# Performance work log

Measured on AMD Instinct MI355X. Metric: run time of the kernel, lower is better.

The kernel has to match this reference:

```python
import jax, jax.numpy as jnp
import numpy as np


def _layernorm(x, w, b):
    mu = x.mean(-1, keepdims=True)
    var = ((x - mu) ** 2).mean(-1, keepdims=True)
    return (x - mu) * jax.lax.rsqrt(var + 1e-5) * w + b


def _s5_scan(u, Lam, Bc, Cc, D, log_step):
    # Diagonal S5 SSM, ZOH discretization, parallel associative scan over time.
    step = jnp.exp(log_step)                       # (P,)
    Lbar = jnp.exp(Lam * step)                     # (P,) complex
    Bbar = ((Lbar - 1.0) / Lam)[:, None] * Bc      # (P,H) complex
    Bu = jnp.einsum('ph,blh->blp', Bbar, u.astype(Bbar.dtype))  # (B,L,P)
    Le = jnp.broadcast_to(Lbar, Bu.shape)

    def binop(e1, e2):
        a1, b1 = e1
        a2, b2 = e2
        return a1 * a2, a2 * b1 + b2

    _, xs = jax.lax.associative_scan(binop, (Le, Bu), axis=1)   # hidden states (B,L,P)
    return 2.0 * jnp.einsum('hp,blp->blh', Cc, xs).real + D * u


def _s5_block(x, ln1_w, ln1_b, Lam_re, Lam_im, B_re, B_im, C_re, C_im, D, log_step,
              ln2_w, ln2_b, ff_enc_w, ff_dec_w):
    # S5Block.forward (dropout = identity at inference)
    fx = _layernorm(x, ln1_w, ln1_b)
    Lam = -jnp.exp(Lam_re) + 1j * Lam_im           # stable-real parametrization
    y = _s5_scan(fx, Lam, B_re + 1j * B_im, C_re + 1j * C_im, D, log_step)
    x = jax.nn.gelu(y, approximate=False) + fx
    fx = _layernorm(x, ln2_w, ln2_b)
    h = fx @ ff_enc_w                              # (B,L,2N) -> GEGLU
    v, g = jnp.split(h, 2, axis=-1)
    h = v * jax.nn.gelu(g, approximate=False)
    return h @ ff_dec_w + fx


def reference(z_input, dt, ln1_w, ln1_b, Lam_re, Lam_im, B_re, B_im, C_re, C_im, D,
              log_step, ln2_w, ln2_b, ff_enc_w, ff_dec_w, toA_w1, toA_b1, toA_w2,
              toA_b2, mask_A):
    Bsz, L, N = z_input.shape
    x = z_input
    for i in range(ln1_w.shape[0]):                # n_ssmlayer_A stacked S5 blocks
        x = _s5_block(x, ln1_w[i], ln1_b[i], Lam_re[i], Lam_im[i], B_re[i], B_im[i],
                      C_re[i], C_im[i], D[i], log_step[i], ln2_w[i], ln2_b[i],
                      ff_enc_w[i], ff_dec_w[i])
    # ssm_to_A: Linear -> Softplus -> Linear
    h = jax.nn.softplus(x @ toA_w1 + toA_b1)
    Unk_A = h @ toA_w2 + toA_b2                    # (B,L,N*N)
    # SSM_step_ODE.get_seq_dynamics with A_known_const = 0
    A = Unk_A.reshape(Bsz, L, N, N) * mask_A
    # bilinear (Tustin) discretization: A_bar = (I - dt/2 A)^-1 (I + dt/2 A)
    I = jnp.eye(N, dtype=A.dtype)
    dtA = 0.5 * dt[..., None, None] * A
    A_bar = jnp.linalg.solve(I - dtA, I + dtA)     # (B,L,N,N)
    # roll latent state through the discretized dynamics
    z0 = z_input[:, 0]

    def step(z, Ab):
        z2 = jnp.einsum('bij,bj->bi', Ab, z)
        return z2, z2

    _, ys = jax.lax.scan(step, z0, jnp.moveaxis(A_bar[:, :-1], 1, 0))
    traj = jnp.concatenate([z0[None], ys], axis=0)  # (L,B,N)
    return jnp.moveaxis(traj, 0, 1)                 # (B,L,N)


def setup_inputs() -> dict:
    key = jax.random.key(0)
    ks = jax.random.split(key, 16)
    B, L, N, P, NL, H = 32, 512, 64, 128, 2, 128
    d = {}
    d['z_input'] = jax.random.normal(ks[0], (B, L, N), jnp.float32)
    d['dt'] = jax.random.uniform(ks[1], (B, L), jnp.float32) * 0.01
    d['ln1_w'] = jnp.ones((NL, N), jnp.float32)
    d['ln1_b'] = jnp.zeros((NL, N), jnp.float32)
    d['Lam_re'] = jax.random.normal(ks[2], (NL, P), jnp.float32) * 0.5
    d['Lam_im'] = jax.random.normal(ks[3], (NL, P), jnp.float32) * np.pi
    d['B_re'] = jax.random.normal(ks[4], (NL, P, N), jnp.float32) / np.sqrt(N)
    d['B_im'] = jax.random.normal(ks[5], (NL, P, N), jnp.float32) / np.sqrt(N)
    d['C_re'] = jax.random.normal(ks[6], (NL, N, P), jnp.float32) / np.sqrt(P)
    d['C_im'] = jax.random.normal(ks[7], (NL, N, P), jnp.float32) / np.sqrt(P)
    d['D'] = jax.random.normal(ks[8], (NL, N), jnp.float32)
    lo, hi = np.log(1e-3), np.log(1e-1)
    d['log_step'] = lo + jax.random.uniform(ks[9], (NL, P), jnp.float32) * (hi - lo)
    d['ln2_w'] = jnp.ones((NL, N), jnp.float32)
    d['ln2_b'] = jnp.zeros((NL, N), jnp.float32)
    d['ff_enc_w'] = jax.random.normal(ks[10], (NL, N, 2 * N), jnp.float32) / np.sqrt(N)
    d['ff_dec_w'] = jax.random.normal(ks[11], (NL, N, N), jnp.float32) / np.sqrt(N)
    d['toA_w1'] = jax.random.normal(ks[12], (N, H), jnp.float32) * 0.1
    d['toA_b1'] = jnp.zeros((H,), jnp.float32)
    d['toA_w2'] = jax.random.normal(ks[13], (H, N * N), jnp.float32) * 0.002
    d['toA_b2'] = jnp.zeros((N * N,), jnp.float32)
    d['mask_A'] = jnp.ones((N, N), jnp.float32)
    return d
```

## Files before the change

### kernel.cpp

```cpp
#include <hip/hip_runtime.h>

#define DI __device__ __forceinline__

typedef unsigned short u16;
typedef unsigned int u32;
typedef __attribute__((ext_vector_type(8))) short shortx8;
typedef __attribute__((ext_vector_type(4))) float floatx4;

DI float u2f(u32 x) { union { u32 u; float f; } v; v.u = x; return v.f; }
DI u32 f2u(float x) { union { u32 u; float f; } v; v.f = x; return v.u; }
DI float bflo(u32 w) { return u2f(w << 16); }
DI float bfhi(u32 w) { return u2f(w & 0xffff0000u); }
DI float bf1(u16 w) { return u2f(((u32)w) << 16); }
DI u16 f2bf(float f) {
  u32 u = f2u(f);
  u32 r = (u + 0x7fffu + ((u >> 16) & 1u)) >> 16;
  return (u16)r;
}

DI float wsum64(float v) {
  v += __shfl_xor(v, 32);
  v += __shfl_xor(v, 16);
  v += __shfl_xor(v, 8);
  v += __shfl_xor(v, 4);
  v += __shfl_xor(v, 2);
  v += __shfl_xor(v, 1);
  return v;
}

DI float gelu_ex(float y) { return 0.5f * y * (1.0f + erff(y * 0.7071067811865476f)); }
DI float softplus_ex(float x) { return x > 0.f ? x + log1pf(expf(-x)) : log1pf(expf(x)); }

__global__ __launch_bounds__(256) void k_pre2(
    const float* __restrict__ Lam_re, const float* __restrict__ Lam_im,
    const float* __restrict__ log_step,
    const float* __restrict__ B_re, const float* __restrict__ B_im,
    const float* __restrict__ C_re, const float* __restrict__ C_im,
    const float* __restrict__ w2,
    float* __restrict__ wLbar, float* __restrict__ wBbr, float* __restrict__ wBbi,
    float* __restrict__ wCtr, float* __restrict__ wCti, u16* __restrict__ w2T) {
  if (blockIdx.x < 64) {
    __shared__ float s[128][65];
    int t = threadIdx.x;
    int n0 = blockIdx.x * 64;
    for (int i = 0; i < 32; ++i) {
      int e = i * 256 + t;
      int k = e >> 6, n = e & 63;
      s[k][n] = w2[(size_t)k * 4096 + n0 + n];
    }
    __syncthreads();
    for (int i = 0; i < 16; ++i) {
      int e = i * 256 + t;
      int n = e >> 6, kp = e & 63;
      u32 pk = (u32)f2bf(s[kp * 2][n]) | ((u32)f2bf(s[kp * 2 + 1][n]) << 16);
      ((u32*)w2T)[(size_t)(n0 + n) * 64 + kp] = pk;
    }
  } else {
    int l = blockIdx.x - 64;
    int p = threadIdx.x;
    if (p < 128) {
      int idx = l * 128 + p;
      float step = expf(log_step[idx]);
      float lre = -expf(Lam_re[idx]);
      float lim = Lam_im[idx];
      float er = expf(lre * step);
      float Lr = er * cosf(lim * step);
      float Li = er * sinf(lim * step);
      wLbar[idx * 2] = Lr;
      wLbar[idx * 2 + 1] = Li;
      float inv = 1.0f / (lre * lre + lim * lim);
      float nr = Lr - 1.0f, ni = Li;
      float qr = (nr * lre + ni * lim) * inv;
      float qi = (ni * lre - nr * lim) * inv;
      for (int h = 0; h < 64; ++h) {
        float br = B_re[idx * 64 + h], bim = B_im[idx * 64 + h];
        wBbr[(l * 64 + h) * 128 + p] = qr * br - qi * bim;
        wBbi[(l * 64 + h) * 128 + p] = qr * bim + qi * br;
        wCtr[idx * 64 + h] = C_re[(l * 64 + h) * 128 + p];
        wCti[idx * 64 + h] = C_im[(l * 64 + h) * 128 + p];
      }
    }
  }
}

__global__ __launch_bounds__(256) void k_ln_bu(
    const float* __restrict__ xin, const float* __restrict__ lnw, const float* __restrict__ lnb,
    const float* __restrict__ wBbr, const float* __restrict__ wBbi,
    float* __restrict__ fxg, float2* __restrict__ bu, int layer) {
  __shared__ float sbr[64 * 128];
  __shared__ float sbi[64 * 128];
  int t = threadIdx.x, w = t >> 6, lane = t & 63;
  {
    const float* br = wBbr + (size_t)layer * 8192;
    const float* bi = wBbi + (size_t)layer * 8192;
    for (int e = t; e < 8192; e += 256) { sbr[e] = br[e]; sbi[e] = bi[e]; }
  }
  float wv = lnw[layer * 64 + lane], bv = lnb[layer * 64 + lane];
  __syncthreads();
  int row0 = blockIdx.x * 32 + w * 8;
  float fxv[8];
#pragma unroll
  for (int rr = 0; rr < 8; ++rr) {
    size_t r = row0 + rr;
    float x = xin[r * 64 + lane];
    float mu = wsum64(x) * 0.015625f;
    float d = x - mu;
    float var = wsum64(d * d) * 0.015625f;
    float fx = d * rsqrtf(var + 1e-5f) * wv + bv;
    fxv[rr] = fx;
    fxg[r * 64 + lane] = fx;
  }
  float ar0[8] = {}, ai0[8] = {}, ar1[8] = {}, ai1[8] = {};
  for (int h = 0; h < 64; ++h) {
    float b0r = sbr[h * 128 + lane], b0i = sbi[h * 128 + lane];
    float b1r = sbr[h * 128 + lane + 64], b1i = sbi[h * 128 + lane + 64];
#pragma unroll
    for (int rr = 0; rr < 8; ++rr) {
      float f = __shfl(fxv[rr], h);
      ar0[rr] = fmaf(b0r, f, ar0[rr]);
      ai0[rr] = fmaf(b0i, f, ai0[rr]);
      ar1[rr] = fmaf(b1r, f, ar1[rr]);
      ai1[rr] = fmaf(b1i, f, ai1[rr]);
    }
  }
#pragma unroll
  for (int rr = 0; rr < 8; ++rr) {
    size_t r = row0 + rr;
    bu[r * 128 + lane] = make_float2(ar0[rr], ai0[rr]);
    bu[r * 128 + lane + 64] = make_float2(ar1[rr], ai1[rr]);
  }
}

__global__ __launch_bounds__(256) void k_scan(float2* __restrict__ bu,
                                              const float* __restrict__ wLbar, int layer) {
  __shared__ float2 carry[16][17];
  int t = threadIdx.x;
  int ck = t >> 4, chain = t & 15;
  int b = blockIdx.x >> 3;
  int p = (blockIdx.x & 7) * 16 + chain;
  float Lr = wLbar[(layer * 128 + p) * 2];
  float Li = wLbar[(layer * 128 + p) * 2 + 1];
  float2* ptr = bu + ((size_t)b * 512 * 128 + p);
  int l0 = ck * 32;
  float xr = 0.f, xi = 0.f;
#pragma unroll 4
  for (int i = 0; i < 32; ++i) {
    float2 v = ptr[(size_t)(l0 + i) * 128];
    float nr = fmaf(Lr, xr, fmaf(-Li, xi, v.x));
    float ni = fmaf(Lr, xi, fmaf(Li, xr, v.y));
    xr = nr; xi = ni;
  }
  carry[chain][ck] = make_float2(xr, xi);
  __syncthreads();
  if (t < 16) {
    float ar = Lr, ai = Li;
#pragma unroll
    for (int s = 0; s < 5; ++s) {
      float nr = ar * ar - ai * ai;
      float ni = 2.f * ar * ai;
      ar = nr; ai = ni;
    }
    float cr = 0.f, ci2 = 0.f;
#pragma unroll
    for (int m = 0; m < 16; ++m) {
      float2 loc = carry[t][m];
      carry[t][m] = make_float2(cr, ci2);
      float nr = fmaf(ar, cr, fmaf(-ai, ci2, loc.x));
      float ni = fmaf(ar, ci2, fmaf(ai, cr, loc.y));
      cr = nr; ci2 = ni;
    }
  }
  __syncthreads();
  float2 c0 = carry[chain][ck];
  xr = c0.x; xi = c0.y;
#pragma unroll 4
  for (int i = 0; i < 32; ++i) {
    float2 v = ptr[(size_t)(l0 + i) * 128];
    float nr = fmaf(Lr, xr, fmaf(-Li, xi, v.x));
    float ni = fmaf(Lr, xi, fmaf(Li, xr, v.y));
    xr = nr; xi = ni;
    ptr[(size_t)(l0 + i) * 128] = make_float2(xr, xi);
  }
}

__global__ __launch_bounds__(256) void k_yff(
    const float2* __restrict__ xs, const float* __restrict__ wCtr, const float* __restrict__ wCti,
    const float* __restrict__ fxg, const float* __restrict__ Dp,
    const float* __restrict__ ln2w, const float* __restrict__ ln2b,
    const float* __restrict__ encw, const float* __restrict__ decw,
    const float* __restrict__ w1, const float* __restrict__ b1,
    float* __restrict__ xout, u16* __restrict__ h1out, int layer) {
  __shared__ union {
    struct { float ctr[4096]; float cti[4096]; float2 xsh[4][8][64]; } a;
    struct { float enc[8192]; float dec[4096]; } b;
    struct { float w1s[8192]; } c;
  } sm;
  int t = threadIdx.x, w = t >> 6, lane = t & 63;
  int row0 = blockIdx.x * 32 + w * 8;
  float acc[8] = {};
  for (int ph = 0; ph < 2; ++ph) {
    __syncthreads();
    {
      const float* sr = wCtr + ((size_t)layer * 128 + ph * 64) * 64;
      const float* si = wCti + ((size_t)layer * 128 + ph * 64) * 64;
      for (int e = t; e < 4096; e += 256) { sm.a.ctr[e] = sr[e]; sm.a.cti[e] = si[e]; }
    }
#pragma unroll
    for (int rr = 0; rr < 8; ++rr) {
      size_t r = row0 + rr;
      sm.a.xsh[w][rr][lane] = xs[r * 128 + ph * 64 + lane];
    }
    __syncthreads();
    for (int p = 0; p < 64; ++p) {
      float cr = sm.a.ctr[p * 64 + lane];
      float ci = sm.a.cti[p * 64 + lane];
#pragma unroll
      for (int rr = 0; rr < 8; ++rr) {
        float2 xv = sm.a.xsh[w][rr][p];
        acc[rr] = fmaf(cr, xv.x, fmaf(-ci, xv.y, acc[rr]));
      }
    }
  }
  float Dv = Dp[layer * 64 + lane];
  float xv[8];
#pragma unroll
  for (int rr = 0; rr < 8; ++rr) {
    size_t r = row0 + rr;
    float u = fxg[r * 64 + lane];
    float y = 2.f * acc[rr] + Dv * u;
    xv[rr] = gelu_ex(y) + u;
  }
  __syncthreads();
  {
    const float* e = encw + (size_t)layer * 8192;
    for (int i = t; i < 8192; i += 256) sm.b.enc[i] = e[i];
    const float* d = decw + (size_t)layer * 4096;
    for (int i = t; i < 4096; i += 256) sm.b.dec[i] = d[i];
  }
  float wv = ln2w[layer * 64 + lane], bv = ln2b[layer * 64 + lane];
  __syncthreads();
  float fx2v[8];
#pragma unroll
  for (int rr = 0; rr < 8; ++rr) {
    float x = xv[rr];
    float mu = wsum64(x) * 0.015625f;
    float d = x - mu;
    float var = wsum64(d * d) * 0.015625f;
    fx2v[rr] = d * rsqrtf(var + 1e-5f) * wv + bv;
  }
  float h0[8] = {}, h1v[8] = {};
  for (int h = 0; h < 64; ++h) {
    float e0 = sm.b.enc[h * 128 + lane], e1 = sm.b.enc[h * 128 + lane + 64];
#pragma unroll
    for (int rr = 0; rr < 8; ++rr) {
      float f = __shfl(fx2v[rr], h);
      h0[rr] = fmaf(e0, f, h0[rr]);
      h1v[rr] = fmaf(e1, f, h1v[rr]);
    }
  }
  float gv[8];
#pragma unroll
  for (int rr = 0; rr < 8; ++rr) gv[rr] = h0[rr] * gelu_ex(h1v[rr]);
  float x2[8];
  {
    float o[8] = {};
    for (int j = 0; j < 64; ++j) {
      float dv = sm.b.dec[j * 64 + lane];
#pragma unroll
      for (int rr = 0; rr < 8; ++rr) {
        float gj = __shfl(gv[rr], j);
        o[rr] = fmaf(dv, gj, o[rr]);
      }
    }
#pragma unroll
    for (int rr = 0; rr < 8; ++rr) x2[rr] = o[rr] + fx2v[rr];
  }
  if (layer == 0) {
#pragma unroll
    for (int rr = 0; rr < 8; ++rr) xout[(size_t)(row0 + rr) * 64 + lane] = x2[rr];
    return;
  }
  __syncthreads();
  for (int i = t; i < 8192; i += 256) sm.c.w1s[i] = w1[i];
  float bb0 = b1[lane], bb1 = b1[lane + 64];
  __syncthreads();
  float a0[8] = {}, a1[8] = {};
  for (int h = 0; h < 64; ++h) {
    float e0 = sm.c.w1s[h * 128 + lane], e1 = sm.c.w1s[h * 128 + lane + 64];
#pragma unroll
    for (int rr = 0; rr < 8; ++rr) {
      float f = __shfl(x2[rr], h);
      a0[rr] = fmaf(e0, f, a0[rr]);
      a1[rr] = fmaf(e1, f, a1[rr]);
    }
  }
#pragma unroll
  for (int rr = 0; rr < 8; ++rr) {
    size_t r = row0 + rr;
    float v0 = softplus_ex(a0[rr] + bb0);
    float v1 = softplus_ex(a1[rr] + bb1);
    int sl = (2 * lane) & 63;
    float ea = __shfl(v0, sl), eb = __shfl(v1, sl);
    float oa = __shfl(v0, sl + 1), ob = __shfl(v1, sl + 1);
    float lo = (lane < 32) ? ea : eb;
    float hi = (lane < 32) ? oa : ob;
    ((u32*)h1out)[r * 64 + lane] = (u32)f2bf(lo) | ((u32)f2bf(hi) << 16);
  }
}

__global__ __launch_bounds__(256) void k_gemm_mfma(
    const u16* __restrict__ w2T, const u16* __restrict__ h1,
    const float* __restrict__ b2, const float* __restrict__ mask,
    const float* __restrict__ dt, u16* __restrict__ Xout) {
  __shared__ __align__(16) u16 As[128 * 128];
  __shared__ __align__(16) u16 Bs[128 * 128];
  int t = threadIdx.x;
  int bn = blockIdx.x;
  int bm = blockIdx.y;
  {
    const u16* srcA = w2T + (size_t)(bn * 128) * 128;
    const u16* srcB = h1 + (size_t)(bm * 128) * 128;
#pragma unroll
    for (int i = 0; i < 8; ++i) {
      int r = i * 16 + (t >> 4);
      int gs = t & 15;
      int gsw = (gs & 8) | ((gs ^ r) & 7);
      uint4 va = *(const uint4*)(srcA + r * 128 + gs * 8);
      *(uint4*)(As + r * 128 + gsw * 8) = va;
      uint4 vb = *(const uint4*)(srcB + r * 128 + gs * 8);
      *(uint4*)(Bs + r * 128 + gsw * 8) = vb;
    }
  }
  __syncthreads();
  int w = t >> 6, l = t & 63;
  int n0 = (w & 1) * 64, m0 = (w >> 1) * 64;
  int lr = l & 15, kg = l >> 4;
  floatx4 acc[4][4];
#pragma unroll
  for (int i = 0; i < 4; ++i)
#pragma unroll
    for (int j = 0; j < 4; ++j) acc[i][j] = (floatx4){0.f, 0.f, 0.f, 0.f};
#pragma unroll
  for (int kk = 0; kk < 4; ++kk) {
    int g = kk * 4 + kg;
    shortx8 af[4], bf[4];
#pragma unroll
    for (int ni = 0; ni < 4; ++ni) {
      int r = n0 + ni * 16 + lr;
      int gsw = (g & 8) | ((g ^ r) & 7);
      af[ni] = *(const shortx8*)(As + r * 128 + gsw * 8);
    }
#pragma unroll
    for (int mi = 0; mi < 4; ++mi) {
      int r = m0 + mi * 16 + lr;
      int gsw = (g & 8) | ((g ^ r) & 7);
      bf[mi] = *(const shortx8*)(Bs + r * 128 + gsw * 8);
    }
#pragma unroll
    for (int ni = 0; ni < 4; ++ni)
#pragma unroll
      for (int mi = 0; mi < 4; ++mi)
        acc[ni][mi] = __builtin_amdgcn_mfma_f32_16x16x32_bf16(af[ni], bf[mi], acc[ni][mi], 0, 0, 0);
  }
  __syncthreads();
  int q = (l >> 4) * 4;
#pragma unroll
  for (int mi = 0; mi < 4; ++mi) {
    int ml = m0 + mi * 16 + lr;
    int m = bm * 128 + ml;
    float dv = 0.5f * dt[m];
#pragma unroll
    for (int ni = 0; ni < 4; ++ni) {
      int nl = n0 + ni * 16 + q;
      int n = bn * 128 + nl;
      float4 bb = *(const float4*)&b2[n];
      float4 mk = *(const float4*)&mask[n];
      floatx4 a = acc[ni][mi];
      float x0 = dv * (a[0] + bb.x) * mk.x;
      float x1 = dv * (a[1] + bb.y) * mk.y;
      float x2 = dv * (a[2] + bb.z) * mk.z;
      float x3 = dv * (a[3] + bb.w) * mk.w;
      u32 lo = (u32)f2bf(x0) | ((u32)f2bf(x1) << 16);
      u32 hi = (u32)f2bf(x2) | ((u32)f2bf(x3) << 16);
      int g = nl >> 3;
      int gsw = (g & 8) | ((g ^ ml) & 7);
      *(uint2*)(As + ml * 128 + gsw * 8 + (nl & 7)) = make_uint2(lo, hi);
    }
  }
  __syncthreads();
  int seg = t & 7;
#pragma unroll
  for (int pp = 0; pp < 4; ++pp) {
    int r = pp * 32 + (t >> 3);
#pragma unroll
    for (int ii = 0; ii < 2; ++ii) {
      int g = seg * 2 + ii;
      int gsw = (g & 8) | ((g ^ r) & 7);
      uint4 v = *(const uint4*)(As + r * 128 + gsw * 8);
      *(uint4*)&Xout[(size_t)(bm * 128 + r) * 4096 + bn * 128 + g * 8] = v;
    }
  }
}

__global__ __launch_bounds__(256, 4) void k_chunk(u16* __restrict__ Xg) {
  __shared__ __align__(16) u16 Xrm[4096];
  __shared__ __align__(16) u16 XTrm[4096];
  __shared__ __align__(16) u16 Erm[4096];
  __shared__ __align__(16) u16 STb[4096];
  __shared__ __align__(16) u16 SOut[4096];
  int t = threadIdx.x, w = t >> 6, l = t & 63;
  int lr = l & 15, kg = l >> 4;
  int b = blockIdx.x >> 5, c = blockIdx.x & 31;
  u16* base = Xg + ((size_t)(b * 512 + c * 16)) * 4096;
  floatx4 sreg[4];
#pragma unroll
  for (int i = 0; i < 4; ++i) sreg[i] = (floatx4){0.f, 0.f, 0.f, 0.f};
  int r0 = (t >> 3) * 2, c0 = (t & 7) * 8, g0 = t & 7;
  int cw = t >> 3;
  uint4 pf0 = *(const uint4*)(base + r0 * 64 + c0);
  uint4 pf1 = *(const uint4*)(base + (r0 + 1) * 64 + c0);
  int q0 = w * 16 + kg * 4;
  int qrow = w * 16 + lr;
  int wr = t >> 2, wg = (t & 3) * 2;
  for (int j = 0; j < 16; ++j) {
    __syncthreads();
    if (j > 0) {
      u16* Xprev = base + (size_t)(j - 1) * 4096;
      uint4 v0 = *(const uint4*)(SOut + wr * 64 + (((wg + 0) ^ wr) & 7) * 8);
      uint4 v1 = *(const uint4*)(SOut + wr * 64 + (((wg + 1) ^ wr) & 7) * 8);
      *(uint4*)(Xprev + wr * 64 + wg * 8) = v0;
      *(uint4*)(Xprev + wr * 64 + wg * 8 + 8) = v1;
    }
    *(uint4*)(Xrm + r0 * 64 + ((g0 ^ r0) & 7) * 8) = pf0;
    *(uint4*)(Xrm + (r0 + 1) * 64 + ((g0 ^ (r0 + 1)) & 7) * 8) = pf1;
    {
      const u16* a = (const u16*)&pf0;
      const u16* bq = (const u16*)&pf1;
#pragma unroll
      for (int i = 0; i < 8; ++i) {
        int ci = (i + t) & 7;
        int cc = c0 + ci;
        u32 val = (u32)a[ci] | ((u32)bq[ci] << 16);
        ((u32*)XTrm)[cc * 32 + (((cw >> 2) ^ cc) & 7) * 4 + (cw & 3)] = val;
      }
    }
#pragma unroll
    for (int j2 = 0; j2 < 4; ++j2) {
      int p = j2 * 16 + lr;
      floatx4 s = sreg[j2];
      float v0 = s[0] + ((p == q0 + 0) ? 1.f : 0.f);
      float v1 = s[1] + ((p == q0 + 1) ? 1.f : 0.f);
      float v2 = s[2] + ((p == q0 + 2) ? 1.f : 0.f);
      float v3 = s[3] + ((p == q0 + 3) ? 1.f : 0.f);
      u32 lo = (u32)f2bf(v0) | ((u32)f2bf(v1) << 16);
      u32 hi = (u32)f2bf(v2) | ((u32)f2bf(v3) << 16);
      *(uint2*)(STb + p * 64 + (((q0 >> 3) ^ p) & 7) * 8 + (q0 & 7)) = make_uint2(lo, hi);
    }
    if (j < 15) {
      const u16* nx = base + (size_t)(j + 1) * 4096;
      pf0 = *(const uint4*)(nx + r0 * 64 + c0);
      pf1 = *(const uint4*)(nx + (r0 + 1) * 64 + c0);
    }
    __syncthreads();
    shortx8 afx0 = *(const shortx8*)(XTrm + qrow * 64 + ((kg ^ qrow) & 7) * 8);
    shortx8 afx1 = *(const shortx8*)(XTrm + qrow * 64 + (((4 + kg) ^ qrow) & 7) * 8);
    {
      floatx4 acc[4];
#pragma unroll
      for (int i = 0; i < 4; ++i) acc[i] = (floatx4){0.f, 0.f, 0.f, 0.f};
#pragma unroll
      for (int kk = 0; kk < 2; ++kk) {
        int g = kk * 4 + kg;
        shortx8 af = kk ? afx1 : afx0;
#pragma unroll
        for (int j2 = 0; j2 < 4; ++j2) {
          int p = j2 * 16 + lr;
          shortx8 bf = *(const shortx8*)(Xrm + p * 64 + ((g ^ p) & 7) * 8);
          acc[j2] = __builtin_amdgcn_mfma_f32_16x16x32_bf16(af, bf, acc[j2], 0, 0, 0);
        }
      }
#pragma unroll
      for (int j2 = 0; j2 < 4; ++j2) {
        int p = j2 * 16 + lr;
        int sw = (((q0 >> 3) ^ p) & 7) * 8 + (q0 & 7);
        uint2 xv = *(const uint2*)(Xrm + p * 64 + sw);
        floatx4 a = acc[j2];
        float e0 = 2.f * (bflo(xv.x) + a[0]);
        float e1 = 2.f * (bfhi(xv.x) + a[1]);
        float e2 = 2.f * (bflo(xv.y) + a[2]);
        float e3 = 2.f * (bfhi(xv.y) + a[3]);
        u32 lo = (u32)f2bf(e0) | ((u32)f2bf(e1) << 16);
        u32 hi = (u32)f2bf(e2) | ((u32)f2bf(e3) << 16);
        *(uint2*)(Erm + p * 64 + sw) = make_uint2(lo, hi);
      }
    }
    __syncthreads();
    {
      floatx4 acc[4];
#pragma unroll
      for (int i = 0; i < 4; ++i) acc[i] = (floatx4){0.f, 0.f, 0.f, 0.f};
#pragma unroll
      for (int kk = 0; kk < 2; ++kk) {
        int g = kk * 4 + kg;
        shortx8 af = *(const shortx8*)(Erm + qrow * 64 + ((g ^ qrow) & 7) * 8);
#pragma unroll
        for (int j2 = 0; j2 < 4; ++j2) {
          int p = j2 * 16 + lr;
          shortx8 bf = *(const shortx8*)(STb + p * 64 + ((g ^ p) & 7) * 8);
          acc[j2] = __builtin_amdgcn_mfma_f32_16x16x32_bf16(af, bf, acc[j2], 0, 0, 0);
        }
      }
#pragma unroll
      for (int j2 = 0; j2 < 4; ++j2) {
        int p = j2 * 16 + lr;
        floatx4 a = acc[j2];
        floatx4 s = sreg[j2];
        s[0] += a[0]; s[1] += a[1]; s[2] += a[2]; s[3] += a[3];
        sreg[j2] = s;
#pragma unroll
        for (int i = 0; i < 4; ++i) {
          int r2 = q0 + i;
          SOut[r2 * 64 + (((p >> 3) ^ r2) & 7) * 8 + (p & 7)] = f2bf(s[i]);
        }
      }
    }
  }
  __syncthreads();
  {
    u16* Xprev = base + (size_t)15 * 4096;
    uint4 v0 = *(const uint4*)(SOut + wr * 64 + (((wg + 0) ^ wr) & 7) * 8);
    uint4 v1 = *(const uint4*)(SOut + wr * 64 + (((wg + 1) ^ wr) & 7) * 8);
    *(uint4*)(Xprev + wr * 64 + wg * 8) = v0;
    *(uint4*)(Xprev + wr * 64 + wg * 8 + 8) = v1;
  }
}

__global__ __launch_bounds__(64) void k_carry(const float* __restrict__ zin,
                                              const u16* __restrict__ R,
                                              float* __restrict__ out) {
  int b = blockIdx.x, l = threadIdx.x;
  uint4 cf[8], nf[8];
  {
    const uint4* M0 = (const uint4*)(R + ((size_t)(b * 512 + 15)) * 4096 + l * 64);
#pragma unroll
    for (int g = 0; g < 8; ++g) cf[g] = M0[g];
  }
  float cz = zin[(size_t)b * 512 * 64 + l];
  for (int c = 0; c < 32; ++c) {
    out[((size_t)(b * 512 + c * 16)) * 64 + l] = cz;
    if (c < 31) {
      const uint4* Mn = (const uint4*)(R + ((size_t)(b * 512 + (c + 1) * 16 + 15)) * 4096 + l * 64);
#pragma unroll
      for (int g = 0; g < 8; ++g) nf[g] = Mn[g];
    }
    float a0 = 0.f, a1 = 0.f, a2 = 0.f, a3 = 0.f;
#pragma unroll
    for (int g = 0; g < 8; ++g) {
      uint4 v = cf[g];
      int k = g * 8;
      a0 = fmaf(bflo(v.x), __shfl(cz, k + 0), a0);
      a1 = fmaf(bfhi(v.x), __shfl(cz, k + 1), a1);
      a2 = fmaf(bflo(v.y), __shfl(cz, k + 2), a2);
      a3 = fmaf(bfhi(v.y), __shfl(cz, k + 3), a3);
      a0 = fmaf(bflo(v.z), __shfl(cz, k + 4), a0);
      a1 = fmaf(bfhi(v.z), __shfl(cz, k + 5), a1);
      a2 = fmaf(bflo(v.w), __shfl(cz, k + 6), a2);
      a3 = fmaf(bfhi(v.w), __shfl(cz, k + 7), a3);
    }
    cz += (a0 + a1) + (a2 + a3);
    if (c < 31) {
#pragma unroll
      for (int g = 0; g < 8; ++g) cf[g] = nf[g];
    }
  }
}

__global__ __launch_bounds__(256) void k_apply(const u16* __restrict__ R,
                                               float* __restrict__ out) {
  __shared__ float carr[64];
  int t = threadIdx.x, w = t >> 6, l = t & 63;
  int b = blockIdx.x >> 5, c = blockIdx.x & 31;
  const u16* Rb = R + ((size_t)(b * 512 + c * 16)) * 4096;
  if (t < 64) carr[t] = out[((size_t)(b * 512 + c * 16)) * 64 + t];
  __syncthreads();
  float zl = carr[l];
  for (int j = w; j < 15; j += 4) {
    const uint4* M = (const uint4*)(Rb + (size_t)j * 4096 + l * 64);
    float a0 = 0.f, a1 = 0.f, a2 = 0.f, a3 = 0.f;
#pragma unroll
    for (int g = 0; g < 8; ++g) {
      uint4 v = M[g];
      const float* zb = &carr[g * 8];
      a0 = fmaf(bflo(v.x), zb[0], a0);
      a1 = fmaf(bfhi(v.x), zb[1], a1);
      a2 = fmaf(bflo(v.y), zb[2], a2);
      a3 = fmaf(bfhi(v.y), zb[3], a3);
      a0 = fmaf(bflo(v.z), zb[4], a0);
      a1 = fmaf(bfhi(v.z), zb[5], a1);
      a2 = fmaf(bflo(v.w), zb[6], a2);
      a3 = fmaf(bfhi(v.w), zb[7], a3);
    }
    out[((size_t)(b * 512 + c * 16 + j + 1)) * 64 + l] = zl + ((a0 + a1) + (a2 + a3));
  }
}

extern "C" void kernel_launch(void* const* d_in, const int* in_sizes, int n_in,
                              void* d_out, int out_size, void* d_ws, size_t ws_size,
                              hipStream_t stream) {
  const float* z_input  = (const float*)d_in[0];
  const float* dt       = (const float*)d_in[1];
  const float* ln1_w    = (const float*)d_in[2];
  const float* ln1_b    = (const float*)d_in[3];
  const float* Lam_re   = (const float*)d_in[4];
  const float* Lam_im   = (const float*)d_in[5];
  const float* B_re     = (const float*)d_in[6];
  const float* B_im     = (const float*)d_in[7];
  const float* C_re     = (const float*)d_in[8];
  const float* C_im     = (const float*)d_in[9];
  const float* Dp       = (const float*)d_in[10];
  const float* log_step = (const float*)d_in[11];
  const float* ln2_w    = (const float*)d_in[12];
  const float* ln2_b    = (const float*)d_in[13];
  const float* ff_enc   = (const float*)d_in[14];
  const float* ff_dec   = (const float*)d_in[15];
  const float* toA_w1   = (const float*)d_in[16];
  const float* toA_b1   = (const float*)d_in[17];
  const float* toA_w2   = (const float*)d_in[18];
  const float* toA_b2   = (const float*)d_in[19];
  const float* mask_A   = (const float*)d_in[20];

  char* ws = (char*)d_ws;
  float* wLbar = (float*)(ws + 0);
  float* wBbr  = (float*)(ws + 2048);
  float* wBbi  = (float*)(ws + 67584);
  float* wCtr  = (float*)(ws + 133120);
  float* wCti  = (float*)(ws + 198656);
  float* wfx   = (float*)(ws + 264192);
  float* wx    = (float*)(ws + 4458496);
  float2* wbu  = (float2*)(ws + 8652800);
  u16* wh1     = (u16*)(ws + 25430016);
  u16* w2T     = (u16*)(ws + 29624320);
  u16* wX      = (u16*)(ws + 30672896);
  if (ws_size < 164890624ull) return;

  k_pre2<<<66, 256, 0, stream>>>(Lam_re, Lam_im, log_step, B_re, B_im, C_re, C_im,
                                 toA_w2, wLbar, wBbr, wBbi, wCtr, wCti, w2T);
  for (int l = 0; l < 2; ++l) {
    const float* xin = (l == 0) ? z_input : wx;
    k_ln_bu<<<512, 256, 0, stream>>>(xin, ln1_w, ln1_b, wBbr, wBbi, wfx, wbu, l);
    k_scan<<<256, 256, 0, stream>>>(wbu, wLbar, l);
    k_yff<<<512, 256, 0, stream>>>(wbu, wCtr, wCti, wfx, Dp, ln2_w, ln2_b, ff_enc, ff_dec,
                                   toA_w1, toA_b1, wx, wh1, l);
  }
  k_gemm_mfma<<<dim3(32, 128), 256, 0, stream>>>(w2T, wh1, toA_b2, mask_A, dt, wX);
  k_chunk<<<1024, 256, 0, stream>>>(wX);
  k_carry<<<32, 64, 0, stream>>>(z_input, wX, (float*)d_out);
  k_apply<<<1024, 256, 0, stream>>>(wX, (float*)d_out);
}
```

Measured before the change: 387.0 us.

## Stop writing per-step chunk prefix matrices; recompute local states sequentially in apply

The chunk kernel now keeps only the final accumulated chunk transition in registers and writes one 64x64 matrix per chunk to a separate buffer, instead of writing all 16 intermediate prefix matrices back over the input. The apply kernel now walks each chunk step by step, applying the original per-step matrices to the carried state with a two-stage update and a shuffle reduction. It drops a shared buffer and raises the occupancy hint. The aim is to cut large global write traffic, at the cost of a serialized, sync-heavy apply loop and a possible change in numerics.

```diff
diff --git a/kernel.cpp b/kernel.cpp
--- a/kernel.cpp
+++ b/kernel.cpp
@@ -402,16 +402,15 @@
   }
 }
 
-__global__ __launch_bounds__(256, 4) void k_chunk(u16* __restrict__ Xg) {
+__global__ __launch_bounds__(256, 5) void k_chunk(const u16* __restrict__ Xg,
+                                                  u16* __restrict__ S15) {
   __shared__ __align__(16) u16 Xrm[4096];
   __shared__ __align__(16) u16 XTrm[4096];
   __shared__ __align__(16) u16 Erm[4096];
   __shared__ __align__(16) u16 STb[4096];
-  __shared__ __align__(16) u16 SOut[4096];
   int t = threadIdx.x, w = t >> 6, l = t & 63;
   int lr = l & 15, kg = l >> 4;
-  int b = blockIdx.x >> 5, c = blockIdx.x & 31;
-  u16* base = Xg + ((size_t)(b * 512 + c * 16)) * 4096;
+  const u16* base = Xg + (size_t)blockIdx.x * 16 * 4096;
   floatx4 sreg[4];
 #pragma unroll
   for (int i = 0; i < 4; ++i) sreg[i] = (floatx4){0.f, 0.f, 0.f, 0.f};
@@ -421,16 +420,8 @@
   uint4 pf1 = *(const uint4*)(base + (r0 + 1) * 64 + c0);
   int q0 = w * 16 + kg * 4;
   int qrow = w * 16 + lr;
-  int wr = t >> 2, wg = (t & 3) * 2;
   for (int j = 0; j < 16; ++j) {
     __syncthreads();
-    if (j > 0) {
-      u16* Xprev = base + (size_t)(j - 1) * 4096;
-      uint4 v0 = *(const uint4*)(SOut + wr * 64 + (((wg + 0) ^ wr) & 7) * 8);
-      uint4 v1 = *(const uint4*)(SOut + wr * 64 + (((wg + 1) ^ wr) & 7) * 8);
-      *(uint4*)(Xprev + wr * 64 + wg * 8) = v0;
-      *(uint4*)(Xprev + wr * 64 + wg * 8 + 8) = v1;
-    }
     *(uint4*)(Xrm + r0 * 64 + ((g0 ^ r0) & 7) * 8) = pf0;
     *(uint4*)(Xrm + (r0 + 1) * 64 + ((g0 ^ (r0 + 1)) & 7) * 8) = pf1;
     {
@@ -512,36 +503,42 @@
       }
 #pragma unroll
       for (int j2 = 0; j2 < 4; ++j2) {
-        int p = j2 * 16 + lr;
         floatx4 a = acc[j2];
         floatx4 s = sreg[j2];
         s[0] += a[0]; s[1] += a[1]; s[2] += a[2]; s[3] += a[3];
         sreg[j2] = s;
-#pragma unroll
-        for (int i = 0; i < 4; ++i) {
-          int r2 = q0 + i;
-          SOut[r2 * 64 + (((p >> 3) ^ r2) & 7) * 8 + (p & 7)] = f2bf(s[i]);
-        }
-      }
+      }
+    }
+  }
+  __syncthreads();
+#pragma unroll
+  for (int j2 = 0; j2 < 4; ++j2) {
+    int p = j2 * 16 + lr;
+    floatx4 s = sreg[j2];
+#pragma unroll
+    for (int i = 0; i < 4; ++i) {
+      int r2 = q0 + i;
+      STb[r2 * 64 + (((p >> 3) ^ r2) & 7) * 8 + (p & 7)] = f2bf(s[i]);
     }
   }
   __syncthreads();
   {
-    u16* Xprev = base + (size_t)15 * 4096;
-    uint4 v0 = *(const uint4*)(SOut + wr * 64 + (((wg + 0) ^ wr) & 7) * 8);
-    uint4 v1 = *(const uint4*)(SOut + wr * 64 + (((wg + 1) ^ wr) & 7) * 8);
-    *(uint4*)(Xprev + wr * 64 + wg * 8) = v0;
-    *(uint4*)(Xprev + wr * 64 + wg * 8 + 8) = v1;
+    u16* dst = S15 + (size_t)blockIdx.x * 4096;
+    int wr = t >> 2, wg = (t & 3) * 2;
+    uint4 v0 = *(const uint4*)(STb + wr * 64 + (((wg + 0) ^ wr) & 7) * 8);
+    uint4 v1 = *(const uint4*)(STb + wr * 64 + (((wg + 1) ^ wr) & 7) * 8);
+    *(uint4*)(dst + wr * 64 + wg * 8) = v0;
+    *(uint4*)(dst + wr * 64 + wg * 8 + 8) = v1;
   }
 }
 
 __global__ __launch_bounds__(64) void k_carry(const float* __restrict__ zin,
-                                              const u16* __restrict__ R,
+                                              const u16* __restrict__ S15,
                                               float* __restrict__ out) {
   int b = blockIdx.x, l = threadIdx.x;
   uint4 cf[8], nf[8];
   {
-    const uint4* M0 = (const uint4*)(R + ((size_t)(b * 512 + 15)) * 4096 + l * 64);
+    const uint4* M0 = (const uint4*)(S15 + (size_t)(b * 32) * 4096 + l * 64);
 #pragma unroll
     for (int g = 0; g < 8; ++g) cf[g] = M0[g];
   }
@@ -549,7 +546,7 @@
   for (int c = 0; c < 32; ++c) {
     out[((size_t)(b * 512 + c * 16)) * 64 + l] = cz;
     if (c < 31) {
-      const uint4* Mn = (const uint4*)(R + ((size_t)(b * 512 + (c + 1) * 16 + 15)) * 4096 + l * 64);
+      const uint4* Mn = (const uint4*)(S15 + (size_t)(b * 32 + c + 1) * 4096 + l * 64);
 #pragma unroll
       for (int g = 0; g < 8; ++g) nf[g] = Mn[g];
     }
@@ -575,32 +572,66 @@
   }
 }
 
-__global__ __launch_bounds__(256) void k_apply(const u16* __restrict__ R,
-                                               float* __restrict__ out) {
-  __shared__ float carr[64];
+DI float dot16(uint4 a0, uint4 a1, const float* zp) {
+  float4 za = *(const float4*)(zp + 0);
+  float4 zb4 = *(const float4*)(zp + 4);
+  float4 zc = *(const float4*)(zp + 8);
+  float4 zd = *(const float4*)(zp + 12);
+  float u = bflo(a0.x) * za.x;
+  u = fmaf(bfhi(a0.x), za.y, u);
+  u = fmaf(bflo(a0.y), za.z, u);
+  u = fmaf(bfhi(a0.y), za.w, u);
+  u = fmaf(bflo(a0.z), zb4.x, u);
+  u = fmaf(bfhi(a0.z), zb4.y, u);
+  u = fmaf(bflo(a0.w), zb4.z, u);
+  u = fmaf(bfhi(a0.w), zb4.w, u);
+  u = fmaf(bflo(a1.x), zc.x, u);
+  u = fmaf(bfhi(a1.x), zc.y, u);
+  u = fmaf(bflo(a1.y), zc.z, u);
+  u = fmaf(bfhi(a1.y), zc.w, u);
+  u = fmaf(bflo(a1.z), zd.x, u);
+  u = fmaf(bfhi(a1.z), zd.y, u);
+  u = fmaf(bflo(a1.w), zd.z, u);
+  u = fmaf(bfhi(a1.w), zd.w, u);
+  return u;
+}
+
+__global__ __launch_bounds__(256) void k_apply2(const u16* __restrict__ X,
+                                                float* __restrict__ out) {
+  __shared__ float zb[64];
+  __shared__ float wb[64];
   int t = threadIdx.x, w = t >> 6, l = t & 63;
   int b = blockIdx.x >> 5, c = blockIdx.x & 31;
-  const u16* Rb = R + ((size_t)(b * 512 + c * 16)) * 4096;
-  if (t < 64) carr[t] = out[((size_t)(b * 512 + c * 16)) * 64 + t];
-  __syncthreads();
-  float zl = carr[l];
-  for (int j = w; j < 15; j += 4) {
-    const uint4* M = (const uint4*)(Rb + (size_t)j * 4096 + l * 64);
-    float a0 = 0.f, a1 = 0.f, a2 = 0.f, a3 = 0.f;
-#pragma unroll
-    for (int g = 0; g < 8; ++g) {
-      uint4 v = M[g];
-      const float* zb = &carr[g * 8];
-      a0 = fmaf(bflo(v.x), zb[0], a0);
-      a1 = fmaf(bfhi(v.x), zb[1], a1);
-      a2 = fmaf(bflo(v.y), zb[2], a2);
-      a3 = fmaf(bfhi(v.y), zb[3], a3);
-      a0 = fmaf(bflo(v.z), zb[4], a0);
-      a1 = fmaf(bfhi(v.z), zb[5], a1);
-      a2 = fmaf(bflo(v.w), zb[6], a2);
-      a3 = fmaf(bfhi(v.w), zb[7], a3);
-    }
-    out[((size_t)(b * 512 + c * 16 + j + 1)) * 64 + l] = zl + ((a0 + a1) + (a2 + a3));
+  const u16* Xb = X + ((size_t)(b * 512 + c * 16)) * 4096;
+  int i = w * 16 + (l >> 2);
+  int kq = l & 3;
+  if (t < 64) zb[t] = out[((size_t)(b * 512 + c * 16)) * 64 + t];
+  const uint4* p0 = (const uint4*)(Xb + i * 64 + kq * 16);
+  uint4 a0 = p0[0], a1 = p0[1];
+  __syncthreads();
+  for (int j = 0; j < 15; ++j) {
+    uint4 n0, n1;
+    if (j < 14) {
+      const uint4* pn = (const uint4*)(Xb + (size_t)(j + 1) * 4096 + i * 64 + kq * 16);
+      n0 = pn[0];
+      n1 = pn[1];
+    }
+    float u = dot16(a0, a1, &zb[kq * 16]);
+    u += __shfl_xor(u, 1);
+    u += __shfl_xor(u, 2);
+    if (kq == 0) wb[i] = zb[i] + u;
+    __syncthreads();
+    float v = dot16(a0, a1, &wb[kq * 16]);
+    v += __shfl_xor(v, 1);
+    v += __shfl_xor(v, 2);
+    if (kq == 0) {
+      float zn = zb[i] + 2.f * v;
+      zb[i] = zn;
+      out[((size_t)(b * 512 + c * 16 + j + 1)) * 64 + i] = zn;
+    }
+    __syncthreads();
+    a0 = n0;
+    a1 = n1;
   }
 }
 
@@ -638,6 +669,7 @@
   float* wfx   = (float*)(ws + 264192);
   float* wx    = (float*)(ws + 4458496);
   float2* wbu  = (float2*)(ws + 8652800);
+  u16* wS15    = (u16*)(ws + 8652800);
   u16* wh1     = (u16*)(ws + 25430016);
   u16* w2T     = (u16*)(ws + 29624320);
   u16* wX      = (u16*)(ws + 30672896);
@@ -653,7 +685,7 @@
                                    toA_w1, toA_b1, wx, wh1, l);
   }
   k_gemm_mfma<<<dim3(32, 128), 256, 0, stream>>>(w2T, wh1, toA_b2, mask_A, dt, wX);
-  k_chunk<<<1024, 256, 0, stream>>>(wX);
-  k_carry<<<32, 64, 0, stream>>>(z_input, wX, (float*)d_out);
-  k_apply<<<1024, 256, 0, stream>>>(wX, (float*)d_out);
-}
+  k_chunk<<<1024, 256, 0, stream>>>(wX, wS15);
+  k_carry<<<32, 64, 0, stream>>>(z_input, wS15, (float*)d_out);
+  k_apply2<<<1024, 256, 0, stream>>>(wX, (float*)d_out);
+}
```

After: 426.0 us. +10.1%, slower.

## Fuse toA GEMM with chunked scan so per-step matrices stay in LDS

Applied to the files above, without the earlier changes.

Merges the large GEMM that builds the per-timestep A matrices with the chunk-scan kernel. Each 512-thread block computes its 16 timesteps' 64x64 matrices straight into LDS and scans them there, so the 128 MB intermediate X is never written to and reread from global memory. Chunk-final states now go to a compact S15 buffer for the carry kernel. The cost is a 160 KB LDS footprint per block (one block per CU), a serial per-block GEMM phase that reloads w2T from global memory for every block, and fewer threads per MFMA tile in the scan.

```diff
diff --git a/kernel.cpp b/kernel.cpp
--- a/kernel.cpp
+++ b/kernel.cpp
@@ -11,7 +11,6 @@
 DI u32 f2u(float x) { union { u32 u; float f; } v; v.f = x; return v.u; }
 DI float bflo(u32 w) { return u2f(w << 16); }
 DI float bfhi(u32 w) { return u2f(w & 0xffff0000u); }
-DI float bf1(u16 w) { return u2f(((u32)w) << 16); }
 DI u16 f2bf(float f) {
   u32 u = f2u(f);
   u32 r = (u + 0x7fffu + ((u >> 16) & 1u)) >> 16;
@@ -308,146 +307,83 @@
   }
 }
 
-__global__ __launch_bounds__(256) void k_gemm_mfma(
-    const u16* __restrict__ w2T, const u16* __restrict__ h1,
+__global__ __launch_bounds__(512, 1) void k_fused(
+    const u16* __restrict__ w2T,
+    const u16* __restrict__ h1,
     const float* __restrict__ b2, const float* __restrict__ mask,
-    const float* __restrict__ dt, u16* __restrict__ Xout) {
-  __shared__ __align__(16) u16 As[128 * 128];
-  __shared__ __align__(16) u16 Bs[128 * 128];
-  int t = threadIdx.x;
-  int bn = blockIdx.x;
-  int bm = blockIdx.y;
-  {
-    const u16* srcA = w2T + (size_t)(bn * 128) * 128;
-    const u16* srcB = h1 + (size_t)(bm * 128) * 128;
-#pragma unroll
-    for (int i = 0; i < 8; ++i) {
-      int r = i * 16 + (t >> 4);
-      int gs = t & 15;
-      int gsw = (gs & 8) | ((gs ^ r) & 7);
-      uint4 va = *(const uint4*)(srcA + r * 128 + gs * 8);
-      *(uint4*)(As + r * 128 + gsw * 8) = va;
-      uint4 vb = *(const uint4*)(srcB + r * 128 + gs * 8);
-      *(uint4*)(Bs + r * 128 + gsw * 8) = vb;
-    }
-  }
-  __syncthreads();
-  int w = t >> 6, l = t & 63;
-  int n0 = (w & 1) * 64, m0 = (w >> 1) * 64;
-  int lr = l & 15, kg = l >> 4;
-  floatx4 acc[4][4];
-#pragma unroll
-  for (int i = 0; i < 4; ++i)
-#pragma unroll
-    for (int j = 0; j < 4; ++j) acc[i][j] = (floatx4){0.f, 0.f, 0.f, 0.f};
-#pragma unroll
-  for (int kk = 0; kk < 4; ++kk) {
-    int g = kk * 4 + kg;
-    shortx8 af[4], bf[4];
-#pragma unroll
-    for (int ni = 0; ni < 4; ++ni) {
-      int r = n0 + ni * 16 + lr;
-      int gsw = (g & 8) | ((g ^ r) & 7);
-      af[ni] = *(const shortx8*)(As + r * 128 + gsw * 8);
-    }
-#pragma unroll
-    for (int mi = 0; mi < 4; ++mi) {
-      int r = m0 + mi * 16 + lr;
-      int gsw = (g & 8) | ((g ^ r) & 7);
-      bf[mi] = *(const shortx8*)(Bs + r * 128 + gsw * 8);
-    }
-#pragma unroll
-    for (int ni = 0; ni < 4; ++ni)
-#pragma unroll
-      for (int mi = 0; mi < 4; ++mi)
-        acc[ni][mi] = __builtin_amdgcn_mfma_f32_16x16x32_bf16(af[ni], bf[mi], acc[ni][mi], 0, 0, 0);
-  }
-  __syncthreads();
-  int q = (l >> 4) * 4;
-#pragma unroll
-  for (int mi = 0; mi < 4; ++mi) {
-    int ml = m0 + mi * 16 + lr;
-    int m = bm * 128 + ml;
-    float dv = 0.5f * dt[m];
-#pragma unroll
-    for (int ni = 0; ni < 4; ++ni) {
-      int nl = n0 + ni * 16 + q;
-      int n = bn * 128 + nl;
-      float4 bb = *(const float4*)&b2[n];
-      float4 mk = *(const float4*)&mask[n];
-      floatx4 a = acc[ni][mi];
-      float x0 = dv * (a[0] + bb.x) * mk.x;
-      float x1 = dv * (a[1] + bb.y) * mk.y;
-      float x2 = dv * (a[2] + bb.z) * mk.z;
-      float x3 = dv * (a[3] + bb.w) * mk.w;
-      u32 lo = (u32)f2bf(x0) | ((u32)f2bf(x1) << 16);
-      u32 hi = (u32)f2bf(x2) | ((u32)f2bf(x3) << 16);
-      int g = nl >> 3;
-      int gsw = (g & 8) | ((g ^ ml) & 7);
-      *(uint2*)(As + ml * 128 + gsw * 8 + (nl & 7)) = make_uint2(lo, hi);
-    }
-  }
-  __syncthreads();
-  int seg = t & 7;
-#pragma unroll
-  for (int pp = 0; pp < 4; ++pp) {
-    int r = pp * 32 + (t >> 3);
-#pragma unroll
-    for (int ii = 0; ii < 2; ++ii) {
-      int g = seg * 2 + ii;
-      int gsw = (g & 8) | ((g ^ r) & 7);
-      uint4 v = *(const uint4*)(As + r * 128 + gsw * 8);
-      *(uint4*)&Xout[(size_t)(bm * 128 + r) * 4096 + bn * 128 + g * 8] = v;
-    }
-  }
-}
-
-__global__ __launch_bounds__(256, 4) void k_chunk(u16* __restrict__ Xg) {
-  __shared__ __align__(16) u16 Xrm[4096];
-  __shared__ __align__(16) u16 XTrm[4096];
-  __shared__ __align__(16) u16 Erm[4096];
+    const float* __restrict__ dt,
+    u16* __restrict__ Sg,
+    u16* __restrict__ S15) {
+  __shared__ __align__(16) u16 Xall[16 * 4096];
+  __shared__ __align__(16) u16 Tb[4096];
   __shared__ __align__(16) u16 STb[4096];
   __shared__ __align__(16) u16 SOut[4096];
-  int t = threadIdx.x, w = t >> 6, l = t & 63;
+  int t = threadIdx.x;
+  int w = t >> 6, l = t & 63;
   int lr = l & 15, kg = l >> 4;
-  int b = blockIdx.x >> 5, c = blockIdx.x & 31;
-  u16* base = Xg + ((size_t)(b * 512 + c * 16)) * 4096;
-  floatx4 sreg[4];
-#pragma unroll
-  for (int i = 0; i < 4; ++i) sreg[i] = (floatx4){0.f, 0.f, 0.f, 0.f};
-  int r0 = (t >> 3) * 2, c0 = (t & 7) * 8, g0 = t & 7;
-  int cw = t >> 3;
-  uint4 pf0 = *(const uint4*)(base + r0 * 64 + c0);
-  uint4 pf1 = *(const uint4*)(base + (r0 + 1) * 64 + c0);
-  int q0 = w * 16 + kg * 4;
-  int qrow = w * 16 + lr;
-  int wr = t >> 2, wg = (t & 3) * 2;
+  int blk = blockIdx.x;
+  int tb = blk * 16;
+
+  float dv = 0.5f * dt[tb + lr];
+  shortx8 bfh[4];
+#pragma unroll
+  for (int kk = 0; kk < 4; ++kk)
+    bfh[kk] = *(const shortx8*)(h1 + (size_t)(tb + lr) * 128 + kk * 32 + kg * 8);
+  for (int it = 0; it < 32; ++it) {
+    int nt = w * 32 + it;
+    floatx4 acc = (floatx4){0.f, 0.f, 0.f, 0.f};
+#pragma unroll
+    for (int kk = 0; kk < 4; ++kk) {
+      shortx8 af = *(const shortx8*)(w2T + (size_t)(nt * 16 + lr) * 128 + kk * 32 + kg * 8);
+      acc = __builtin_amdgcn_mfma_f32_16x16x32_bf16(af, bfh[kk], acc, 0, 0, 0);
+    }
+    int n0 = nt * 16 + kg * 4;
+    float4 bb = *(const float4*)&b2[n0];
+    float4 mk = *(const float4*)&mask[n0];
+    float x0 = dv * (acc[0] + bb.x) * mk.x;
+    float x1 = dv * (acc[1] + bb.y) * mk.y;
+    float x2 = dv * (acc[2] + bb.z) * mk.z;
+    float x3 = dv * (acc[3] + bb.w) * mk.w;
+    u32 lo = (u32)f2bf(x0) | ((u32)f2bf(x1) << 16);
+    u32 hi = (u32)f2bf(x2) | ((u32)f2bf(x3) << 16);
+    int p = n0 >> 6, q = n0 & 63;
+    int gsw = ((q >> 3) ^ p ^ lr) & 7;
+    *(uint2*)(Xall + lr * 4096 + p * 64 + gsw * 8 + (q & 7)) = make_uint2(lo, hi);
+  }
+
+  int qt = w >> 1, pt0 = (w & 1) * 2;
+  int qrow = qt * 16 + lr;
+  int q0 = qt * 16 + kg * 4;
+  floatx4 sreg[2];
+  sreg[0] = (floatx4){0.f, 0.f, 0.f, 0.f};
+  sreg[1] = (floatx4){0.f, 0.f, 0.f, 0.f};
+  int r0 = (t >> 4) * 2, c0 = (t & 15) * 4, cw = t >> 4;
+  int wr = t >> 3, wg = t & 7;
   for (int j = 0; j < 16; ++j) {
     __syncthreads();
     if (j > 0) {
-      u16* Xprev = base + (size_t)(j - 1) * 4096;
-      uint4 v0 = *(const uint4*)(SOut + wr * 64 + (((wg + 0) ^ wr) & 7) * 8);
-      uint4 v1 = *(const uint4*)(SOut + wr * 64 + (((wg + 1) ^ wr) & 7) * 8);
-      *(uint4*)(Xprev + wr * 64 + wg * 8) = v0;
-      *(uint4*)(Xprev + wr * 64 + wg * 8 + 8) = v1;
-    }
-    *(uint4*)(Xrm + r0 * 64 + ((g0 ^ r0) & 7) * 8) = pf0;
-    *(uint4*)(Xrm + (r0 + 1) * 64 + ((g0 ^ (r0 + 1)) & 7) * 8) = pf1;
+      u16* dst = Sg + (size_t)(tb + j - 1) * 4096;
+      uint4 v = *(const uint4*)(SOut + wr * 64 + ((wg ^ wr) & 7) * 8);
+      *(uint4*)(dst + wr * 64 + wg * 8) = v;
+    }
     {
-      const u16* a = (const u16*)&pf0;
-      const u16* bq = (const u16*)&pf1;
-#pragma unroll
-      for (int i = 0; i < 8; ++i) {
-        int ci = (i + t) & 7;
+      const u16* Xj = Xall + j * 4096;
+      uint2 a = *(const uint2*)(Xj + r0 * 64 + (((c0 >> 3) ^ r0 ^ j) & 7) * 8 + (c0 & 7));
+      uint2 b = *(const uint2*)(Xj + (r0 + 1) * 64 + (((c0 >> 3) ^ (r0 + 1) ^ j) & 7) * 8 + (c0 & 7));
+      const u16* au = (const u16*)&a;
+      const u16* bu2 = (const u16*)&b;
+#pragma unroll
+      for (int i = 0; i < 4; ++i) {
+        int ci = (i + t) & 3;
         int cc = c0 + ci;
-        u32 val = (u32)a[ci] | ((u32)bq[ci] << 16);
-        ((u32*)XTrm)[cc * 32 + (((cw >> 2) ^ cc) & 7) * 4 + (cw & 3)] = val;
-      }
-    }
-#pragma unroll
-    for (int j2 = 0; j2 < 4; ++j2) {
-      int p = j2 * 16 + lr;
-      floatx4 s = sreg[j2];
+        u32 val = (u32)au[ci] | ((u32)bu2[ci] << 16);
+        ((u32*)Tb)[cc * 32 + (((cw >> 2) ^ cc) & 7) * 4 + (cw & 3)] = val;
+      }
+    }
+#pragma unroll
+    for (int i = 0; i < 2; ++i) {
+      int p = (pt0 + i) * 16 + lr;
+      floatx4 s = sreg[i];
       float v0 = s[0] + ((p == q0 + 0) ? 1.f : 0.f);
       float v1 = s[1] + ((p == q0 + 1) ? 1.f : 0.f);
       float v2 = s[2] + ((p == q0 + 2) ? 1.f : 0.f);
@@ -456,92 +392,89 @@
       u32 hi = (u32)f2bf(v2) | ((u32)f2bf(v3) << 16);
       *(uint2*)(STb + p * 64 + (((q0 >> 3) ^ p) & 7) * 8 + (q0 & 7)) = make_uint2(lo, hi);
     }
-    if (j < 15) {
-      const u16* nx = base + (size_t)(j + 1) * 4096;
-      pf0 = *(const uint4*)(nx + r0 * 64 + c0);
-      pf1 = *(const uint4*)(nx + (r0 + 1) * 64 + c0);
-    }
-    __syncthreads();
-    shortx8 afx0 = *(const shortx8*)(XTrm + qrow * 64 + ((kg ^ qrow) & 7) * 8);
-    shortx8 afx1 = *(const shortx8*)(XTrm + qrow * 64 + (((4 + kg) ^ qrow) & 7) * 8);
+    __syncthreads();
+    float ev[2][4];
     {
-      floatx4 acc[4];
-#pragma unroll
-      for (int i = 0; i < 4; ++i) acc[i] = (floatx4){0.f, 0.f, 0.f, 0.f};
+      shortx8 afx0 = *(const shortx8*)(Tb + qrow * 64 + ((kg ^ qrow) & 7) * 8);
+      shortx8 afx1 = *(const shortx8*)(Tb + qrow * 64 + (((4 + kg) ^ qrow) & 7) * 8);
+      floatx4 acc[2];
+      acc[0] = (floatx4){0.f, 0.f, 0.f, 0.f};
+      acc[1] = (floatx4){0.f, 0.f, 0.f, 0.f};
 #pragma unroll
       for (int kk = 0; kk < 2; ++kk) {
         int g = kk * 4 + kg;
         shortx8 af = kk ? afx1 : afx0;
 #pragma unroll
-        for (int j2 = 0; j2 < 4; ++j2) {
-          int p = j2 * 16 + lr;
-          shortx8 bf = *(const shortx8*)(Xrm + p * 64 + ((g ^ p) & 7) * 8);
-          acc[j2] = __builtin_amdgcn_mfma_f32_16x16x32_bf16(af, bf, acc[j2], 0, 0, 0);
+        for (int i = 0; i < 2; ++i) {
+          int p = (pt0 + i) * 16 + lr;
+          shortx8 bf = *(const shortx8*)(Xall + j * 4096 + p * 64 + ((g ^ p ^ j) & 7) * 8);
+          acc[i] = __builtin_amdgcn_mfma_f32_16x16x32_bf16(af, bf, acc[i], 0, 0, 0);
         }
       }
 #pragma unroll
-      for (int j2 = 0; j2 < 4; ++j2) {
-        int p = j2 * 16 + lr;
-        int sw = (((q0 >> 3) ^ p) & 7) * 8 + (q0 & 7);
-        uint2 xv = *(const uint2*)(Xrm + p * 64 + sw);
-        floatx4 a = acc[j2];
-        float e0 = 2.f * (bflo(xv.x) + a[0]);
-        float e1 = 2.f * (bfhi(xv.x) + a[1]);
-        float e2 = 2.f * (bflo(xv.y) + a[2]);
-        float e3 = 2.f * (bfhi(xv.y) + a[3]);
-        u32 lo = (u32)f2bf(e0) | ((u32)f2bf(e1) << 16);
-        u32 hi = (u32)f2bf(e2) | ((u32)f2bf(e3) << 16);
-        *(uint2*)(Erm + p * 64 + sw) = make_uint2(lo, hi);
-      }
+      for (int i = 0; i < 2; ++i) {
+        int p = (pt0 + i) * 16 + lr;
+        uint2 xv = *(const uint2*)(Xall + j * 4096 + p * 64 + (((q0 >> 3) ^ p ^ j) & 7) * 8 + (q0 & 7));
+        ev[i][0] = 2.f * (bflo(xv.x) + acc[i][0]);
+        ev[i][1] = 2.f * (bfhi(xv.x) + acc[i][1]);
+        ev[i][2] = 2.f * (bflo(xv.y) + acc[i][2]);
+        ev[i][3] = 2.f * (bfhi(xv.y) + acc[i][3]);
+      }
+    }
+    __syncthreads();
+#pragma unroll
+    for (int i = 0; i < 2; ++i) {
+      int p = (pt0 + i) * 16 + lr;
+      u32 lo = (u32)f2bf(ev[i][0]) | ((u32)f2bf(ev[i][1]) << 16);
+      u32 hi = (u32)f2bf(ev[i][2]) | ((u32)f2bf(ev[i][3]) << 16);
+      *(uint2*)(Tb + p * 64 + (((q0 >> 3) ^ p) & 7) * 8 + (q0 & 7)) = make_uint2(lo, hi);
     }
     __syncthreads();
     {
-      floatx4 acc[4];
-#pragma unroll
-      for (int i = 0; i < 4; ++i) acc[i] = (floatx4){0.f, 0.f, 0.f, 0.f};
+      shortx8 ae0 = *(const shortx8*)(Tb + qrow * 64 + ((kg ^ qrow) & 7) * 8);
+      shortx8 ae1 = *(const shortx8*)(Tb + qrow * 64 + (((4 + kg) ^ qrow) & 7) * 8);
+      floatx4 acc[2];
+      acc[0] = (floatx4){0.f, 0.f, 0.f, 0.f};
+      acc[1] = (floatx4){0.f, 0.f, 0.f, 0.f};
 #pragma unroll
       for (int kk = 0; kk < 2; ++kk) {
         int g = kk * 4 + kg;
-        shortx8 af = *(const shortx8*)(Erm + qrow * 64 + ((g ^ qrow) & 7) * 8);
-#pragma unroll
-        for (int j2 = 0; j2 < 4; ++j2) {
-          int p = j2 * 16 + lr;
+        shortx8 af = kk ? ae1 : ae0;
+#pragma unroll
+        for (int i = 0; i < 2; ++i) {
+          int p = (pt0 + i) * 16 + lr;
           shortx8 bf = *(const shortx8*)(STb + p * 64 + ((g ^ p) & 7) * 8);
-          acc[j2] = __builtin_amdgcn_mfma_f32_16x16x32_bf16(af, bf, acc[j2], 0, 0, 0);
+          acc[i] = __builtin_amdgcn_mfma_f32_16x16x32_bf16(af, bf, acc[i], 0, 0, 0);
         }
       }
 #pragma unroll
-      for (int j2 = 0; j2 < 4; ++j2) {
-        int p = j2 * 16 + lr;
-        floatx4 a = acc[j2];
-        floatx4 s = sreg[j2];
-        s[0] += a[0]; s[1] += a[1]; s[2] += a[2]; s[3] += a[3];
-        sreg[j2] = s;
-#pragma unroll
-        for (int i = 0; i < 4; ++i) {
-          int r2 = q0 + i;
-          SOut[r2 * 64 + (((p >> 3) ^ r2) & 7) * 8 + (p & 7)] = f2bf(s[i]);
+      for (int i = 0; i < 2; ++i) {
+        floatx4 s = sreg[i];
+        s[0] += acc[i][0]; s[1] += acc[i][1]; s[2] += acc[i][2]; s[3] += acc[i][3];
+        sreg[i] = s;
+        int p = (pt0 + i) * 16 + lr;
+#pragma unroll
+        for (int ii = 0; ii < 4; ++ii) {
+          int r2 = q0 + ii;
+          SOut[r2 * 64 + (((p >> 3) ^ r2) & 7) * 8 + (p & 7)] = f2bf(s[ii]);
         }
       }
     }
   }
   __syncthreads();
   {
-    u16* Xprev = base + (size_t)15 * 4096;
-    uint4 v0 = *(const uint4*)(SOut + wr * 64 + (((wg + 0) ^ wr) & 7) * 8);
-    uint4 v1 = *(const uint4*)(SOut + wr * 64 + (((wg + 1) ^ wr) & 7) * 8);
-    *(uint4*)(Xprev + wr * 64 + wg * 8) = v0;
-    *(uint4*)(Xprev + wr * 64 + wg * 8 + 8) = v1;
+    uint4 v = *(const uint4*)(SOut + wr * 64 + ((wg ^ wr) & 7) * 8);
+    *(uint4*)(S15 + (size_t)blk * 4096 + wr * 64 + wg * 8) = v;
   }
 }
 
 __global__ __launch_bounds__(64) void k_carry(const float* __restrict__ zin,
-                                              const u16* __restrict__ R,
+                                              const u16* __restrict__ S15,
                                               float* __restrict__ out) {
   int b = blockIdx.x, l = threadIdx.x;
   uint4 cf[8], nf[8];
   {
-    const uint4* M0 = (const uint4*)(R + ((size_t)(b * 512 + 15)) * 4096 + l * 64);
+    const uint4* M0 = (const uint4*)(S15 + (size_t)(b * 32) * 4096 + l * 64);
 #pragma unroll
     for (int g = 0; g < 8; ++g) cf[g] = M0[g];
   }
@@ -549,7 +482,7 @@
   for (int c = 0; c < 32; ++c) {
     out[((size_t)(b * 512 + c * 16)) * 64 + l] = cz;
     if (c < 31) {
-      const uint4* Mn = (const uint4*)(R + ((size_t)(b * 512 + (c + 1) * 16 + 15)) * 4096 + l * 64);
+      const uint4* Mn = (const uint4*)(S15 + (size_t)(b * 32 + c + 1) * 4096 + l * 64);
 #pragma unroll
       for (int g = 0; g < 8; ++g) nf[g] = Mn[g];
     }
@@ -638,9 +571,10 @@
   float* wfx   = (float*)(ws + 264192);
   float* wx    = (float*)(ws + 4458496);
   float2* wbu  = (float2*)(ws + 8652800);
+  u16* wS15    = (u16*)(ws + 8652800);
   u16* wh1     = (u16*)(ws + 25430016);
   u16* w2T     = (u16*)(ws + 29624320);
-  u16* wX      = (u16*)(ws + 30672896);
+  u16* wS      = (u16*)(ws + 30672896);
   if (ws_size < 164890624ull) return;
 
   k_pre2<<<66, 256, 0, stream>>>(Lam_re, Lam_im, log_step, B_re, B_im, C_re, C_im,
@@ -652,8 +586,7 @@
     k_yff<<<512, 256, 0, stream>>>(wbu, wCtr, wCti, wfx, Dp, ln2_w, ln2_b, ff_enc, ff_dec,
                                    toA_w1, toA_b1, wx, wh1, l);
   }
-  k_gemm_mfma<<<dim3(32, 128), 256, 0, stream>>>(w2T, wh1, toA_b2, mask_A, dt, wX);
-  k_chunk<<<1024, 256, 0, stream>>>(wX);
-  k_carry<<<32, 64, 0, stream>>>(z_input, wX, (float*)d_out);
-  k_apply<<<1024, 256, 0, stream>>>(wX, (float*)d_out);
-}
+  k_fused<<<1024, 512, 0, stream>>>(w2T, wh1, toA_b2, mask_A, dt, wS, wS15);
+  k_carry<<<32, 64, 0, stream>>>(z_input, wS15, (float*)d_out);
+  k_apply<<<1024, 256, 0, stream>>>(wS, (float*)d_out);
+}
```

After: 483.3 us. +24.9%, slower.
